# Performance work log

Hardware: AMD Instinct MI355X
Metric: run time of the kernel (lower is better)

## Reference

```python
import jax, jax.numpy as jnp
import numpy as np

DIM = 384
HEADS = 6
K = 10          # default k of DynamicGraphAttention
HID = 1536      # int(dim * mlp_ratio)
LN_EPS = 1e-5


def layernorm(x, g, b):
    m = jnp.mean(x, -1, keepdims=True)
    var = jnp.mean((x - m) ** 2, -1, keepdims=True)
    return (x - m) * jax.lax.rsqrt(var + LN_EPS) * g + b


def setup_inputs() -> dict:
    key = jax.random.key(0)
    ks = jax.random.split(key, 12)
    B, N, M, C = 16, 1024, 512, DIM
    s = 0.02
    return dict(
        q=jax.random.normal(ks[0], (B, N, C), jnp.float32),
        v=jax.random.normal(ks[1], (B, M, C), jnp.float32),
        q_pos=jax.random.normal(ks[2], (B, N, 3), jnp.float32),
        v_pos=jax.random.normal(ks[3], (B, M, 3), jnp.float32),
        norm1_g=jnp.ones((C,), jnp.float32), norm1_b=jnp.zeros((C,), jnp.float32),
        qkv_w=jax.random.normal(ks[4], (C, 3 * C), jnp.float32) * s,  # qkv_bias=False
        proj_w=jax.random.normal(ks[5], (C, C), jnp.float32) * s,
        proj_b=jnp.zeros((C,), jnp.float32),
        normq_g=jnp.ones((C,), jnp.float32), normq_b=jnp.zeros((C,), jnp.float32),
        normv_g=jnp.ones((C,), jnp.float32), normv_b=jnp.zeros((C,), jnp.float32),
        knn_w=jax.random.normal(ks[6], (2 * C, C), jnp.float32) * s,
        knn_b=jnp.zeros((C,), jnp.float32),
        norm2_g=jnp.ones((C,), jnp.float32), norm2_b=jnp.zeros((C,), jnp.float32),
        fc1_w=jax.random.normal(ks[7], (C, HID), jnp.float32) * s,
        fc1_b=jnp.zeros((HID,), jnp.float32),
        fc2_w=jax.random.normal(ks[8], (HID, C), jnp.float32) * s,
        fc2_b=jnp.zeros((C,), jnp.float32),
    )


def reference(q, v, q_pos, v_pos,
              norm1_g, norm1_b, qkv_w, proj_w, proj_b,
              normq_g, normq_b, normv_g, normv_b, knn_w, knn_b,
              norm2_g, norm2_b, fc1_w, fc1_b, fc2_w, fc2_b):
    B, N, C = q.shape
    D = C // HEADS

    # --- multi-head self-attention with pre-norm residual ---
    x = layernorm(q, norm1_g, norm1_b)
    qkv = (x @ qkv_w).reshape(B, N, 3, HEADS, D)
    qh, kh, vh = qkv[:, :, 0], qkv[:, :, 1], qkv[:, :, 2]   # [B,N,H,D]
    attn = jnp.einsum('bnhd,bmhd->bhnm', qh, kh) * (D ** -0.5)
    attn = jax.nn.softmax(attn, axis=-1)
    sa = jnp.einsum('bhnm,bmhd->bnhd', attn, vh).reshape(B, N, C)
    sa = sa @ proj_w + proj_b
    q = q + sa

    # --- dynamic graph cross-attention (knn gather + diff-concat MLP + max) ---
    nq = layernorm(q, normq_g, normq_b)          # [B,N,C]
    nv = layernorm(v, normv_g, normv_b)          # [B,M,C]
    # squared distances between query and kv positions: [B,N,M]
    d = (jnp.sum(q_pos ** 2, -1)[:, :, None]
         + jnp.sum(v_pos ** 2, -1)[:, None, :]
         - 2.0 * jnp.einsum('bnc,bmc->bnm', q_pos, v_pos))
    _, idx = jax.lax.top_k(-d, K)                # K nearest neighbors, [B,N,K]
    local_v = jax.vmap(lambda vv, ii: vv[ii])(nv, idx)   # [B,N,K,C]
    qe = nq[:, :, None, :]                                # [B,N,1,C]
    feat = jnp.concatenate(
        [local_v - qe, jnp.broadcast_to(qe, local_v.shape)], axis=-1)  # [B,N,K,2C]
    g = jax.nn.leaky_relu(feat @ knn_w + knn_b, negative_slope=0.2)
    q = q + jnp.max(g, axis=-2)                  # max over K neighbors

    # --- MLP with pre-norm residual ---
    h = layernorm(q, norm2_g, norm2_b)
    h = jax.nn.gelu(h @ fc1_w + fc1_b, approximate=False)
    h = h @ fc2_w + fc2_b
    return q + h
```

## Files before the change

kernel.cpp:

```cpp
#include <hip/hip_runtime.h>
#include <hip/hip_bf16.h>

#define CDIM 384
#define NHEAD 6
#define DHEAD 64
#define BB 16
#define NQ 1024
#define MV 512
#define HIDD 1536
#define KNN 10

typedef __attribute__((ext_vector_type(8))) __bf16 bf16x8;
typedef __attribute__((ext_vector_type(4))) float f32x4;
typedef __attribute__((ext_vector_type(4))) short short4v;

__device__ inline void ln_row(const float* __restrict__ xr, const float* __restrict__ gw,
                              const float* __restrict__ bw, __hip_bfloat16* __restrict__ outr,
                              int lane) {
  float v0[6];
  float s = 0.f;
#pragma unroll
  for (int i = 0; i < 3; i++) {
    float2 t = *reinterpret_cast<const float2*>(xr + i * 128 + lane * 2);
    v0[i * 2] = t.x; v0[i * 2 + 1] = t.y; s += t.x + t.y;
  }
  for (int off = 32; off; off >>= 1) s += __shfl_xor(s, off);
  float mean = s * (1.f / 384.f);
  float sq = 0.f;
#pragma unroll
  for (int i = 0; i < 6; i++) { float d = v0[i] - mean; sq += d * d; }
  for (int off = 32; off; off >>= 1) sq += __shfl_xor(sq, off);
  float rstd = rsqrtf(sq * (1.f / 384.f) + 1e-5f);
#pragma unroll
  for (int i = 0; i < 3; i++) {
    int c = i * 128 + lane * 2;
    float2 gg = *reinterpret_cast<const float2*>(gw + c);
    float2 bb = *reinterpret_cast<const float2*>(bw + c);
    __hip_bfloat162 p;
    p.x = __float2bfloat16((v0[i * 2] - mean) * rstd * gg.x + bb.x);
    p.y = __float2bfloat16((v0[i * 2 + 1] - mean) * rstd * gg.y + bb.y);
    *reinterpret_cast<__hip_bfloat162*>(outr + c) = p;
  }
}

__global__ __launch_bounds__(256) void prep_kernel(
    const float* __restrict__ qkv_w, const float* __restrict__ proj_w,
    const float* __restrict__ knn_w, const float* __restrict__ fc1_w,
    const float* __restrict__ fc2_w, const float* __restrict__ q,
    const float* __restrict__ g1, const float* __restrict__ b1,
    __hip_bfloat16* __restrict__ Wqkv_t, __hip_bfloat16* __restrict__ Wproj_t,
    __hip_bfloat16* __restrict__ W1_t, __hip_bfloat16* __restrict__ Wd_t,
    __hip_bfloat16* __restrict__ Wfc1_t, __hip_bfloat16* __restrict__ Wfc2_t,
    __hip_bfloat16* __restrict__ Xbf) {
  int gid = blockIdx.x;
  if (gid >= 1872) {
    int wave = (gid - 1872) * 4 + ((int)threadIdx.x >> 6);
    int lane = threadIdx.x & 63;
    ln_row(q + (size_t)wave * CDIM, g1, b1, Xbf + (size_t)wave * CDIM, lane);
    return;
  }
  __shared__ float t1[32][33];
  __shared__ float t2[32][33];
  int tx = threadIdx.x & 31, ty = (int)threadIdx.x >> 5;
  if (gid >= 576 && gid < 720) {
    int id = gid - 576;
    int k0 = (id % 12) * 32, n0 = (id / 12) * 32;
#pragma unroll
    for (int i = 0; i < 4; i++) {
      int k = k0 + ty + i * 8;
      float w1 = knn_w[(size_t)k * CDIM + n0 + tx];
      float w2 = knn_w[(size_t)(CDIM + k) * CDIM + n0 + tx];
      t1[ty + i * 8][tx] = w1;
      t2[ty + i * 8][tx] = w2 - w1;
    }
    __syncthreads();
#pragma unroll
    for (int i = 0; i < 4; i++) {
      W1_t[(size_t)(n0 + ty + i * 8) * CDIM + k0 + tx] = __float2bfloat16(t1[tx][ty + i * 8]);
      Wd_t[(size_t)(n0 + ty + i * 8) * CDIM + k0 + tx] = __float2bfloat16(t2[tx][ty + i * 8]);
    }
    return;
  }
  const float* W;
  __hip_bfloat16* Wt;
  int Kd, Nd, k0, n0;
  if (gid < 432) {
    W = qkv_w; Wt = Wqkv_t; Kd = 384; Nd = 1152;
    k0 = (gid % 12) * 32; n0 = (gid / 12) * 32;
  } else if (gid < 576) {
    int id = gid - 432;
    W = proj_w; Wt = Wproj_t; Kd = 384; Nd = 384;
    k0 = (id % 12) * 32; n0 = (id / 12) * 32;
  } else if (gid < 1296) {
    int id = gid - 720;
    W = fc1_w; Wt = Wfc1_t; Kd = 384; Nd = 1536;
    k0 = (id % 12) * 32; n0 = (id / 12) * 32;
  } else {
    int id = gid - 1296;
    W = fc2_w; Wt = Wfc2_t; Kd = 1536; Nd = 384;
    k0 = (id % 48) * 32; n0 = (id / 48) * 32;
  }
#pragma unroll
  for (int i = 0; i < 4; i++)
    t1[ty + i * 8][tx] = W[(size_t)(k0 + ty + i * 8) * Nd + n0 + tx];
  __syncthreads();
#pragma unroll
  for (int i = 0; i < 4; i++)
    Wt[(size_t)(n0 + ty + i * 8) * Kd + k0 + tx] = __float2bfloat16(t1[tx][ty + i * 8]);
}

__global__ __launch_bounds__(256) void ln_dual_kernel(const float* __restrict__ q1,
                                                      const float* __restrict__ v,
                                                      const float* __restrict__ gq,
                                                      const float* __restrict__ bq,
                                                      const float* __restrict__ gv,
                                                      const float* __restrict__ bv,
                                                      __hip_bfloat16* __restrict__ Xbf,
                                                      __hip_bfloat16* __restrict__ NV) {
  int wave = (int)((blockIdx.x * blockDim.x + threadIdx.x) >> 6);
  int lane = threadIdx.x & 63;
  if (wave < BB * NQ) {
    ln_row(q1 + (size_t)wave * CDIM, gq, bq, Xbf + (size_t)wave * CDIM, lane);
  } else {
    int r = wave - BB * NQ;
    ln_row(v + (size_t)r * CDIM, gv, bv, NV + (size_t)r * CDIM, lane);
  }
}

template <int EPI, int BM>
__global__ __launch_bounds__(256) void gemm_kernel(const __hip_bfloat16* __restrict__ A,
                                                   const __hip_bfloat16* __restrict__ Bt,
                                                   const float* __restrict__ bias,
                                                   const float* __restrict__ resid,
                                                   void* __restrict__ outp,
                                                   void* __restrict__ out2,
                                                   void* __restrict__ out3,
                                                   int M, int N, int Kdim) {
  constexpr int MI = BM / 32;
  constexpr int STAGEB = BM * 64 * 2 + 128 * 64 * 2;
  constexpr int SMEMB = (EPI == 5) ? (128 * 136 * 2 > STAGEB ? 128 * 136 * 2 : STAGEB) : STAGEB;
  __shared__ __align__(16) char smem[SMEMB];
  char* AsB = smem;
  char* BsB = smem + BM * 64 * 2;
  int m0 = blockIdx.y * BM, n0 = blockIdx.x * 128;
  const __hip_bfloat16* Ause = A;
  const __hip_bfloat16* Bt_use = Bt;
  bool isA1 = false;
  if (EPI == 6) {
    constexpr int A2B = 16384 / BM;
    if ((int)blockIdx.y >= A2B) {
      isA1 = true;
      m0 = (blockIdx.y - A2B) * BM;
      Ause = (const __hip_bfloat16*)out3;
    } else {
      Bt_use = Bt + (size_t)384 * 384;
    }
  }
  int t = threadIdx.x;
  int lane = t & 63, w = t >> 6;
  int wrow = w >> 1, wcol = w & 1;
  int lg = lane >> 4, lr = lane & 15;
  int gcol = (((lane & 7) ^ (lane >> 3)) * 8);
  const __hip_bfloat16* Ab = Ause + (size_t)(m0 + w * 8 + (lane >> 3)) * Kdim + gcol;
  const __hip_bfloat16* Bb = Bt_use + (size_t)(n0 + w * 8 + (lane >> 3)) * Kdim + gcol;
  f32x4 acc[MI][4] = {};
  for (int k0 = 0; k0 < Kdim; k0 += 64) {
    if (k0) __syncthreads();
#pragma unroll
    for (int i = 0; i < MI; i++)
      __builtin_amdgcn_global_load_lds(
          (const __attribute__((address_space(1))) void*)(Ab + (size_t)(i * 32) * Kdim + k0),
          (__attribute__((address_space(3))) void*)(AsB + (i * 4 + w) * 1024), 16, 0, 0);
#pragma unroll
    for (int i = 0; i < 4; i++)
      __builtin_amdgcn_global_load_lds(
          (const __attribute__((address_space(1))) void*)(Bb + (size_t)(i * 32) * Kdim + k0),
          (__attribute__((address_space(3))) void*)(BsB + (i * 4 + w) * 1024), 16, 0, 0);
    __syncthreads();
#pragma unroll
    for (int kk = 0; kk < 2; kk++) {
      bf16x8 a[MI], b[4];
#pragma unroll
      for (int i = 0; i < MI; i++) {
        int ra = wrow * (BM / 2) + i * 16 + lr;
        int sw = (((kk << 2) | lg) ^ (lr & 7)) * 16;
        a[i] = *reinterpret_cast<const bf16x8*>(AsB + ra * 128 + sw);
      }
#pragma unroll
      for (int j = 0; j < 4; j++) {
        int rb = wcol * 64 + j * 16 + lr;
        int sw = (((kk << 2) | lg) ^ (lr & 7)) * 16;
        b[j] = *reinterpret_cast<const bf16x8*>(BsB + rb * 128 + sw);
      }
#pragma unroll
      for (int i = 0; i < MI; i++)
#pragma unroll
        for (int j = 0; j < 4; j++)
          acc[i][j] = __builtin_amdgcn_mfma_f32_16x16x32_bf16(a[i], b[j], acc[i][j], 0, 0, 0);
    }
  }
  if (EPI == 5 && blockIdx.x >= 6) {
    __syncthreads();
    __hip_bfloat16* S = (__hip_bfloat16*)smem;
#pragma unroll
    for (int i = 0; i < MI; i++)
#pragma unroll
      for (int j = 0; j < 4; j++) {
        int lc = wcol * 64 + j * 16 + lr;
#pragma unroll
        for (int r = 0; r < 4; r++) {
          int lrow = wrow * 64 + i * 16 + lg * 4 + r;
          S[lc * 136 + lrow] = __float2bfloat16(acc[i][j][r]);
        }
      }
    __syncthreads();
    int b = m0 >> 10, nbase = m0 & 1023;
    int lc = t >> 1, half = t & 1;
    int c = n0 + lc - 2 * CDIM;
    int h = c >> 6, d = c & 63;
    __hip_bfloat16* dst = (__hip_bfloat16*)out3 +
                          ((size_t)((b * NHEAD + h) * DHEAD + d)) * NQ + nbase + half * 64;
#pragma unroll
    for (int u = 0; u < 8; u++)
      *reinterpret_cast<uint4*>(dst + u * 8) =
          *reinterpret_cast<const uint4*>(&S[lc * 136 + half * 64 + u * 8]);
    return;
  }
#pragma unroll
  for (int i = 0; i < MI; i++)
#pragma unroll
    for (int j = 0; j < 4; j++) {
      int col = n0 + wcol * 64 + j * 16 + lr;
#pragma unroll
      for (int r = 0; r < 4; r++) {
        int row = m0 + wrow * (BM / 2) + i * 16 + lg * 4 + r;
        float v = acc[i][j][r];
        if (EPI == 5) {
          int b = row >> 10, n = row & 1023;
          if (col < CDIM) {
            int h = col >> 6, d = col & 63;
            ((__hip_bfloat16*)outp)[(((size_t)(b * NHEAD + h)) * NQ + n) * DHEAD + d] =
                __float2bfloat16(v * 0.18033688f);
          } else {
            int c = col - CDIM, h = c >> 6, d = c & 63;
            ((__hip_bfloat16*)out2)[(((size_t)(b * NHEAD + h)) * NQ + n) * DHEAD + d] =
                __float2bfloat16(v);
          }
        } else if (EPI == 6) {
          float vv = v;
          if (!isA1) vv += bias[col];
          float* dst = isA1 ? (float*)out2 : (float*)outp;
          dst[(size_t)row * 384 + col] = vv;
        } else {
          if (EPI == 1 || EPI == 2 || EPI == 3) v += bias[col];
          if (EPI == 2) v += resid[(size_t)row * N + col];
          if (EPI == 3) v = 0.5f * v * (1.f + erff(v * 0.70710678118654752f));
          if (EPI == 0 || EPI == 3)
            ((__hip_bfloat16*)outp)[(size_t)row * N + col] = __float2bfloat16(v);
          else
            ((float*)outp)[(size_t)row * N + col] = v;
        }
      }
    }
}

__global__ __launch_bounds__(256) void attn_kernel(const __hip_bfloat16* __restrict__ Qb,
                                                   const __hip_bfloat16* __restrict__ Kb,
                                                   const __hip_bfloat16* __restrict__ Vt,
                                                   __hip_bfloat16* __restrict__ SAb) {
  __shared__ __align__(16) __hip_bfloat16 Ks[2][64][72];
  __shared__ __align__(16) __hip_bfloat16 Vs[2][64][72];
  int bh = blockIdx.x % 96;
  int qblk = blockIdx.x / 96;
  int t = threadIdx.x;
  int w = t >> 6, lane = t & 63;
  int lg = lane >> 4, lr = lane & 15;
  const __hip_bfloat16* Qp = Qb + (size_t)bh * NQ * DHEAD;
  const __hip_bfloat16* Kp = Kb + (size_t)bh * NQ * DHEAD;
  const __hip_bfloat16* Vp = Vt + (size_t)bh * DHEAD * NQ;
  int q0 = qblk * 128 + w * 32;
  bf16x8 qf[2][2];
#pragma unroll
  for (int qt = 0; qt < 2; qt++)
#pragma unroll
    for (int kk = 0; kk < 2; kk++)
      qf[qt][kk] = *reinterpret_cast<const bf16x8*>(
          Qp + (size_t)(q0 + qt * 16 + lr) * DHEAD + kk * 32 + lg * 8);
  int srow = w * 16 + (lane >> 2);
  int scol = (lane & 3) * 16;
  uint4 kr0 = *reinterpret_cast<const uint4*>(Kp + (size_t)srow * DHEAD + scol);
  uint4 kr1 = *reinterpret_cast<const uint4*>(Kp + (size_t)srow * DHEAD + scol + 8);
  uint4 vr0 = *reinterpret_cast<const uint4*>(Vp + (size_t)srow * NQ + scol);
  uint4 vr1 = *reinterpret_cast<const uint4*>(Vp + (size_t)srow * NQ + scol + 8);
  *reinterpret_cast<uint4*>(&Ks[0][srow][scol]) = kr0;
  *reinterpret_cast<uint4*>(&Ks[0][srow][scol + 8]) = kr1;
  *reinterpret_cast<uint4*>(&Vs[0][srow][scol]) = vr0;
  *reinterpret_cast<uint4*>(&Vs[0][srow][scol + 8]) = vr1;
  f32x4 o[2][4] = {};
  float l_[2] = {0.f, 0.f};
  __syncthreads();
  for (int kt = 0; kt < 16; kt++) {
    int cur = kt & 1;
    if (kt < 15) {
      int kb = (kt + 1) * 64;
      kr0 = *reinterpret_cast<const uint4*>(Kp + (size_t)(kb + srow) * DHEAD + scol);
      kr1 = *reinterpret_cast<const uint4*>(Kp + (size_t)(kb + srow) * DHEAD + scol + 8);
      vr0 = *reinterpret_cast<const uint4*>(Vp + (size_t)srow * NQ + kb + scol);
      vr1 = *reinterpret_cast<const uint4*>(Vp + (size_t)srow * NQ + kb + scol + 8);
    }
    f32x4 s[4][2] = {};
#pragma unroll
    for (int kti = 0; kti < 4; kti++)
#pragma unroll
      for (int kk = 0; kk < 2; kk++) {
        bf16x8 a = *reinterpret_cast<const bf16x8*>(&Ks[cur][kti * 16 + lr][kk * 32 + lg * 8]);
#pragma unroll
        for (int qt = 0; qt < 2; qt++)
          s[kti][qt] = __builtin_amdgcn_mfma_f32_16x16x32_bf16(a, qf[qt][kk], s[kti][qt], 0, 0, 0);
      }
#pragma unroll
    for (int qt = 0; qt < 2; qt++) {
      float ls = 0.f;
#pragma unroll
      for (int kti = 0; kti < 4; kti++) {
        float p0 = __builtin_amdgcn_exp2f(s[kti][qt][0]);
        float p1 = __builtin_amdgcn_exp2f(s[kti][qt][1]);
        float p2 = __builtin_amdgcn_exp2f(s[kti][qt][2]);
        float p3 = __builtin_amdgcn_exp2f(s[kti][qt][3]);
        s[kti][qt][0] = p0; s[kti][qt][1] = p1; s[kti][qt][2] = p2; s[kti][qt][3] = p3;
        ls += (p0 + p1) + (p2 + p3);
      }
      l_[qt] += ls;
    }
#pragma unroll
    for (int kti = 0; kti < 4; kti++) {
      short4v pa[2];
#pragma unroll
      for (int qt = 0; qt < 2; qt++) {
#pragma unroll
        for (int r = 0; r < 4; r++) {
          __bf16 hv = (__bf16)s[kti][qt][r];
          pa[qt][r] = __builtin_bit_cast(short, hv);
        }
      }
#pragma unroll
      for (int dt = 0; dt < 4; dt++) {
        short4v vb = *reinterpret_cast<const short4v*>(&Vs[cur][dt * 16 + lr][kti * 16 + lg * 4]);
#pragma unroll
        for (int qt = 0; qt < 2; qt++)
          o[qt][dt] = __builtin_amdgcn_mfma_f32_16x16x16bf16_1k(pa[qt], vb, o[qt][dt], 0, 0, 0);
      }
    }
    if (kt < 15) {
      int nb = cur ^ 1;
      *reinterpret_cast<uint4*>(&Ks[nb][srow][scol]) = kr0;
      *reinterpret_cast<uint4*>(&Ks[nb][srow][scol + 8]) = kr1;
      *reinterpret_cast<uint4*>(&Vs[nb][srow][scol]) = vr0;
      *reinterpret_cast<uint4*>(&Vs[nb][srow][scol + 8]) = vr1;
      __syncthreads();
    }
  }
#pragma unroll
  for (int qt = 0; qt < 2; qt++) {
    l_[qt] += __shfl_xor(l_[qt], 16);
    l_[qt] += __shfl_xor(l_[qt], 32);
  }
  int b = bh / NHEAD, h = bh % NHEAD;
#pragma unroll
  for (int qt = 0; qt < 2; qt++)
#pragma unroll
    for (int r = 0; r < 4; r++) {
      float li = __shfl(l_[qt], (lane & 48) | (((lane >> 4) & 3) * 4 + r));
      float inv = 1.f / li;
      int row = q0 + qt * 16 + ((lane >> 4) & 3) * 4 + r;
#pragma unroll
      for (int dt = 0; dt < 4; dt++)
        SAb[((size_t)(b * NQ + row)) * CDIM + h * DHEAD + dt * 16 + lr] =
            __float2bfloat16(o[qt][dt][r] * inv);
    }
}

__global__ __launch_bounds__(256) void knn_fused_kernel(const float* __restrict__ q_pos,
                                                        const float* __restrict__ v_pos,
                                                        const float* __restrict__ A1,
                                                        const float* __restrict__ A2,
                                                        const float* __restrict__ q1,
                                                        const float* __restrict__ g2,
                                                        const float* __restrict__ b2,
                                                        float* __restrict__ q2,
                                                        __hip_bfloat16* __restrict__ xout) {
  int wq = (int)((blockIdx.x * blockDim.x + threadIdx.x) >> 6);
  int lane = threadIdx.x & 63;
  if (wq >= BB * NQ) return;
  int b = wq >> 10;
  const float* qp = q_pos + (size_t)wq * 3;
  float qx = qp[0], qy = qp[1], qz = qp[2];
  float qs = qx * qx + qy * qy + qz * qz;
  unsigned long long pk[8];
#pragma unroll
  for (int j = 0; j < 8; j++) {
    int m = lane + 64 * j;
    const float* vp = v_pos + ((size_t)b * MV + m) * 3;
    float vx = vp[0], vy = vp[1], vz = vp[2];
    float vs = vx * vx + vy * vy + vz * vz;
    float d = qs + vs - 2.f * (qx * vx + qy * vy + qz * vz);
    unsigned ub = __float_as_uint(d);
    ub ^= (unsigned)(((int)ub >> 31)) | 0x80000000u;
    pk[j] = ((unsigned long long)ub << 32) | (unsigned)m;
  }
  unsigned long long lm = pk[0];
#pragma unroll
  for (int j = 1; j < 8; j++) lm = pk[j] < lm ? pk[j] : lm;
  int idxs[KNN];
#pragma unroll
  for (int k = 0; k < KNN; k++) {
    unsigned long long bm = lm;
#pragma unroll
    for (int off = 1; off < 64; off <<= 1) {
      unsigned long long ot = __shfl_xor(bm, off);
      bm = ot < bm ? ot : bm;
    }
    int widx = (int)(unsigned)(bm & 0xFFFFFFFFull);
    idxs[k] = widx;
    if ((widx & 63) == lane) {
      int jj = widx >> 6;
#pragma unroll
      for (int j = 0; j < 8; j++)
        if (j == jj) pk[j] = ~0ull;
      lm = pk[0];
#pragma unroll
      for (int j = 1; j < 8; j++) lm = pk[j] < lm ? pk[j] : lm;
    }
  }
  float a2[6], mx[6];
#pragma unroll
  for (int i = 0; i < 6; i++) {
    a2[i] = A2[(size_t)wq * CDIM + lane + 64 * i];
    mx[i] = -1e30f;
  }
#pragma unroll
  for (int k = 0; k < KNN; k++) {
    const float* a1 = A1 + ((size_t)b * MV + idxs[k]) * CDIM;
#pragma unroll
    for (int i = 0; i < 6; i++) {
      float g = a1[lane + 64 * i] + a2[i];
      g = g > 0.f ? g : 0.2f * g;
      mx[i] = fmaxf(mx[i], g);
    }
  }
  float vals[6];
  float s = 0.f;
#pragma unroll
  for (int i = 0; i < 6; i++) {
    vals[i] = q1[(size_t)wq * CDIM + lane + 64 * i] + mx[i];
    s += vals[i];
  }
  for (int off = 32; off; off >>= 1) s += __shfl_xor(s, off);
  float mean = s * (1.f / 384.f);
  float sq = 0.f;
#pragma unroll
  for (int i = 0; i < 6; i++) { float d = vals[i] - mean; sq += d * d; }
  for (int off = 32; off; off >>= 1) sq += __shfl_xor(sq, off);
  float rstd = rsqrtf(sq * (1.f / 384.f) + 1e-5f);
#pragma unroll
  for (int i = 0; i < 6; i++) {
    int c = lane + 64 * i;
    q2[(size_t)wq * CDIM + c] = vals[i];
    xout[(size_t)wq * CDIM + c] = __float2bfloat16((vals[i] - mean) * rstd * g2[c] + b2[c]);
  }
}

extern "C" void kernel_launch(void* const* d_in, const int* in_sizes, int n_in,
                              void* d_out, int out_size, void* d_ws, size_t ws_size,
                              hipStream_t stream) {
  const float* q = (const float*)d_in[0];
  const float* v = (const float*)d_in[1];
  const float* q_pos = (const float*)d_in[2];
  const float* v_pos = (const float*)d_in[3];
  const float* norm1_g = (const float*)d_in[4];
  const float* norm1_b = (const float*)d_in[5];
  const float* qkv_w = (const float*)d_in[6];
  const float* proj_w = (const float*)d_in[7];
  const float* proj_b = (const float*)d_in[8];
  const float* normq_g = (const float*)d_in[9];
  const float* normq_b = (const float*)d_in[10];
  const float* normv_g = (const float*)d_in[11];
  const float* normv_b = (const float*)d_in[12];
  const float* knn_w = (const float*)d_in[13];
  const float* knn_b = (const float*)d_in[14];
  const float* norm2_g = (const float*)d_in[15];
  const float* norm2_b = (const float*)d_in[16];
  const float* fc1_w = (const float*)d_in[17];
  const float* fc1_b = (const float*)d_in[18];
  const float* fc2_w = (const float*)d_in[19];
  const float* fc2_b = (const float*)d_in[20];

  char* ws = (char*)d_ws;
  const size_t SZ_Wqkv = (size_t)1152 * 384 * 2;
  const size_t SZ_W384 = (size_t)384 * 384 * 2;
  const size_t SZ_Wfc = (size_t)1536 * 384 * 2;
  const size_t SZ_Xbf = (size_t)16384 * 384 * 2;
  const size_t SZ_QKV = (size_t)16384 * 1152 * 2;
  const size_t SZ_q32 = (size_t)16384 * 384 * 4;
  const size_t SZ_NV = (size_t)8192 * 384 * 2;

  size_t o_Wqkv = 0;
  size_t o_Wproj = o_Wqkv + SZ_Wqkv;
  size_t o_W1 = o_Wproj + SZ_W384;
  size_t o_Wd = o_W1 + SZ_W384;
  size_t o_Wfc1 = o_Wd + SZ_W384;
  size_t o_Wfc2 = o_Wfc1 + SZ_Wfc;
  size_t o_Xbf = o_Wfc2 + SZ_Wfc;
  size_t o_QKV = o_Xbf + SZ_Xbf;
  size_t o_A1 = o_QKV;
  size_t o_A2 = o_QKV + (size_t)8192 * 384 * 4;
  size_t o_Qb = o_QKV + SZ_QKV;
  size_t o_Kb = o_Qb + SZ_Xbf;
  size_t o_Vt = o_Kb + SZ_Xbf;
  size_t o_SA = o_Vt + SZ_Xbf;
  size_t o_H1 = o_Qb;
  size_t o_q1 = o_SA + SZ_Xbf;
  size_t o_NV = o_q1 + SZ_q32;
  size_t o_q2 = o_NV + SZ_NV;

  __hip_bfloat16* Wqkv_t = (__hip_bfloat16*)(ws + o_Wqkv);
  __hip_bfloat16* Wproj_t = (__hip_bfloat16*)(ws + o_Wproj);
  __hip_bfloat16* W1_t = (__hip_bfloat16*)(ws + o_W1);
  __hip_bfloat16* Wd_t = (__hip_bfloat16*)(ws + o_Wd);
  __hip_bfloat16* Wfc1_t = (__hip_bfloat16*)(ws + o_Wfc1);
  __hip_bfloat16* Wfc2_t = (__hip_bfloat16*)(ws + o_Wfc2);
  __hip_bfloat16* Xbf = (__hip_bfloat16*)(ws + o_Xbf);
  float* A1f = (float*)(ws + o_A1);
  float* A2f = (float*)(ws + o_A2);
  __hip_bfloat16* Qb = (__hip_bfloat16*)(ws + o_Qb);
  __hip_bfloat16* Kb = (__hip_bfloat16*)(ws + o_Kb);
  __hip_bfloat16* Vt = (__hip_bfloat16*)(ws + o_Vt);
  __hip_bfloat16* SAb = (__hip_bfloat16*)(ws + o_SA);
  __hip_bfloat16* H1 = (__hip_bfloat16*)(ws + o_H1);
  float* q1 = (float*)(ws + o_q1);
  __hip_bfloat16* NV = (__hip_bfloat16*)(ws + o_NV);
  float* q2 = (float*)(ws + o_q2);
  float* outf = (float*)d_out;

  prep_kernel<<<5968, 256, 0, stream>>>(qkv_w, proj_w, knn_w, fc1_w, fc2_w, q,
                                        norm1_g, norm1_b,
                                        Wqkv_t, Wproj_t, W1_t, Wd_t, Wfc1_t, Wfc2_t, Xbf);
  gemm_kernel<5, 128><<<dim3(9, 128), 256, 0, stream>>>(Xbf, Wqkv_t, nullptr, nullptr,
                                                        Qb, Kb, Vt, 16384, 1152, 384);
  attn_kernel<<<768, 256, 0, stream>>>(Qb, Kb, Vt, SAb);
  gemm_kernel<2, 64><<<dim3(3, 256), 256, 0, stream>>>(SAb, Wproj_t, proj_b, q, q1,
                                                       nullptr, nullptr, 16384, 384, 384);
  ln_dual_kernel<<<6144, 256, 0, stream>>>(q1, v, normq_g, normq_b, normv_g, normv_b, Xbf, NV);
  gemm_kernel<6, 64><<<dim3(3, 384), 256, 0, stream>>>(Xbf, W1_t, knn_b, nullptr, A2f,
                                                       A1f, (void*)NV, 16384, 384, 384);
  knn_fused_kernel<<<4096, 256, 0, stream>>>(q_pos, v_pos, A1f, A2f, q1,
                                             norm2_g, norm2_b, q2, Xbf);
  gemm_kernel<3, 128><<<dim3(12, 128), 256, 0, stream>>>(Xbf, Wfc1_t, fc1_b, nullptr, H1,
                                                         nullptr, nullptr, 16384, 1536, 384);
  gemm_kernel<2, 64><<<dim3(3, 256), 256, 0, stream>>>(H1, Wfc2_t, fc2_b, q2, outf,
                                                       nullptr, nullptr, 16384, 384, 1536);
}
```

Before: 270.4 us.

## Move kNN top-k, value layernorm and neighbour GEMM into earlier kernels

The kNN distance computation and top-k selection now run as extra blocks in the prep kernel, which writes the indices to a workspace buffer that the fused kNN kernel reads back. The value-side layernorm also moves into the prep kernel. The nv@W1 GEMM moves into the QKV GEMM launch as extra grid rows, so only the query-side GEMM is left after the residual. The aim is to put work that does not depend on the attention output onto earlier, larger launches, and to shorten the serial chain after attention. The cost is an extra index buffer round trip through global memory and a larger prep grid with mixed block roles.

```diff
diff --git a/kernel.cpp b/kernel.cpp
--- a/kernel.cpp
+++ b/kernel.cpp
@@ -48,11 +48,64 @@
     const float* __restrict__ knn_w, const float* __restrict__ fc1_w,
     const float* __restrict__ fc2_w, const float* __restrict__ q,
     const float* __restrict__ g1, const float* __restrict__ b1,
+    const float* __restrict__ v, const float* __restrict__ gv, const float* __restrict__ bv,
+    const float* __restrict__ q_pos, const float* __restrict__ v_pos,
     __hip_bfloat16* __restrict__ Wqkv_t, __hip_bfloat16* __restrict__ Wproj_t,
     __hip_bfloat16* __restrict__ W1_t, __hip_bfloat16* __restrict__ Wd_t,
     __hip_bfloat16* __restrict__ Wfc1_t, __hip_bfloat16* __restrict__ Wfc2_t,
-    __hip_bfloat16* __restrict__ Xbf) {
+    __hip_bfloat16* __restrict__ Xbf, __hip_bfloat16* __restrict__ NV,
+    int* __restrict__ idxb) {
   int gid = blockIdx.x;
+  if (gid >= 8016) {
+    int wq = (gid - 8016) * 4 + ((int)threadIdx.x >> 6);
+    int lane = threadIdx.x & 63;
+    int b = wq >> 10;
+    const float* qp = q_pos + (size_t)wq * 3;
+    float qx = qp[0], qy = qp[1], qz = qp[2];
+    float qs = qx * qx + qy * qy + qz * qz;
+    unsigned long long pk[8];
+#pragma unroll
+    for (int j = 0; j < 8; j++) {
+      int m = lane + 64 * j;
+      const float* vp = v_pos + ((size_t)b * MV + m) * 3;
+      float vx = vp[0], vy = vp[1], vz = vp[2];
+      float vs = vx * vx + vy * vy + vz * vz;
+      float d = qs + vs - 2.f * (qx * vx + qy * vy + qz * vz);
+      unsigned ub = __float_as_uint(d);
+      ub ^= (unsigned)(((int)ub >> 31)) | 0x80000000u;
+      pk[j] = ((unsigned long long)ub << 32) | (unsigned)m;
+    }
+    unsigned long long lm = pk[0];
+#pragma unroll
+    for (int j = 1; j < 8; j++) lm = pk[j] < lm ? pk[j] : lm;
+#pragma unroll
+    for (int k = 0; k < KNN; k++) {
+      unsigned long long bm = lm;
+#pragma unroll
+      for (int off = 1; off < 64; off <<= 1) {
+        unsigned long long ot = __shfl_xor(bm, off);
+        bm = ot < bm ? ot : bm;
+      }
+      int widx = (int)(unsigned)(bm & 0xFFFFFFFFull);
+      if (lane == 0) idxb[wq * KNN + k] = widx;
+      if ((widx & 63) == lane) {
+        int jj = widx >> 6;
+#pragma unroll
+        for (int j = 0; j < 8; j++)
+          if (j == jj) pk[j] = ~0ull;
+        lm = pk[0];
+#pragma unroll
+        for (int j = 1; j < 8; j++) lm = pk[j] < lm ? pk[j] : lm;
+      }
+    }
+    return;
+  }
+  if (gid >= 5968) {
+    int row = (gid - 5968) * 4 + ((int)threadIdx.x >> 6);
+    int lane = threadIdx.x & 63;
+    ln_row(v + (size_t)row * CDIM, gv, bv, NV + (size_t)row * CDIM, lane);
+    return;
+  }
   if (gid >= 1872) {
     int wave = (gid - 1872) * 4 + ((int)threadIdx.x >> 6);
     int lane = threadIdx.x & 63;
@@ -109,22 +162,14 @@
     Wt[(size_t)(n0 + ty + i * 8) * Kd + k0 + tx] = __float2bfloat16(t1[tx][ty + i * 8]);
 }
 
-__global__ __launch_bounds__(256) void ln_dual_kernel(const float* __restrict__ q1,
-                                                      const float* __restrict__ v,
-                                                      const float* __restrict__ gq,
-                                                      const float* __restrict__ bq,
-                                                      const float* __restrict__ gv,
-                                                      const float* __restrict__ bv,
-                                                      __hip_bfloat16* __restrict__ Xbf,
-                                                      __hip_bfloat16* __restrict__ NV) {
+__global__ __launch_bounds__(256) void ln_kernel(const float* __restrict__ x,
+                                                 const float* __restrict__ gw,
+                                                 const float* __restrict__ bw,
+                                                 __hip_bfloat16* __restrict__ out, int rows) {
   int wave = (int)((blockIdx.x * blockDim.x + threadIdx.x) >> 6);
   int lane = threadIdx.x & 63;
-  if (wave < BB * NQ) {
-    ln_row(q1 + (size_t)wave * CDIM, gq, bq, Xbf + (size_t)wave * CDIM, lane);
-  } else {
-    int r = wave - BB * NQ;
-    ln_row(v + (size_t)r * CDIM, gv, bv, NV + (size_t)r * CDIM, lane);
-  }
+  if (wave >= rows) return;
+  ln_row(x + (size_t)wave * CDIM, gw, bw, out + (size_t)wave * CDIM, lane);
 }
 
 template <int EPI, int BM>
@@ -146,6 +191,15 @@
   const __hip_bfloat16* Ause = A;
   const __hip_bfloat16* Bt_use = Bt;
   bool isA1 = false;
+  if (EPI == 5) {
+    if ((int)blockIdx.y >= 128) {
+      if ((int)blockIdx.x >= 3) return;
+      isA1 = true;
+      m0 = (blockIdx.y - 128) * 128;
+      Ause = (const __hip_bfloat16*)bias;
+      Bt_use = Bt + (size_t)(1152 * 384 + 384 * 384);
+    }
+  }
   if (EPI == 6) {
     constexpr int A2B = 16384 / BM;
     if ((int)blockIdx.y >= A2B) {
@@ -199,7 +253,7 @@
           acc[i][j] = __builtin_amdgcn_mfma_f32_16x16x32_bf16(a[i], b[j], acc[i][j], 0, 0, 0);
     }
   }
-  if (EPI == 5 && blockIdx.x >= 6) {
+  if (EPI == 5 && !isA1 && blockIdx.x >= 6) {
     __syncthreads();
     __hip_bfloat16* S = (__hip_bfloat16*)smem;
 #pragma unroll
@@ -236,15 +290,19 @@
         int row = m0 + wrow * (BM / 2) + i * 16 + lg * 4 + r;
         float v = acc[i][j][r];
         if (EPI == 5) {
-          int b = row >> 10, n = row & 1023;
-          if (col < CDIM) {
-            int h = col >> 6, d = col & 63;
-            ((__hip_bfloat16*)outp)[(((size_t)(b * NHEAD + h)) * NQ + n) * DHEAD + d] =
-                __float2bfloat16(v * 0.18033688f);
+          if (isA1) {
+            ((float*)(size_t)resid)[(size_t)row * 384 + col] = v;
           } else {
-            int c = col - CDIM, h = c >> 6, d = c & 63;
-            ((__hip_bfloat16*)out2)[(((size_t)(b * NHEAD + h)) * NQ + n) * DHEAD + d] =
-                __float2bfloat16(v);
+            int b = row >> 10, n = row & 1023;
+            if (col < CDIM) {
+              int h = col >> 6, d = col & 63;
+              ((__hip_bfloat16*)outp)[(((size_t)(b * NHEAD + h)) * NQ + n) * DHEAD + d] =
+                  __float2bfloat16(v * 0.18033688f);
+            } else {
+              int c = col - CDIM, h = c >> 6, d = c & 63;
+              ((__hip_bfloat16*)out2)[(((size_t)(b * NHEAD + h)) * NQ + n) * DHEAD + d] =
+                  __float2bfloat16(v);
+            }
           }
         } else if (EPI == 6) {
           float vv = v;
@@ -380,8 +438,7 @@
     }
 }
 
-__global__ __launch_bounds__(256) void knn_fused_kernel(const float* __restrict__ q_pos,
-                                                        const float* __restrict__ v_pos,
+__global__ __launch_bounds__(256) void knn_fused_kernel(const int* __restrict__ idxb,
                                                         const float* __restrict__ A1,
                                                         const float* __restrict__ A2,
                                                         const float* __restrict__ q1,
@@ -393,45 +450,9 @@
   int lane = threadIdx.x & 63;
   if (wq >= BB * NQ) return;
   int b = wq >> 10;
-  const float* qp = q_pos + (size_t)wq * 3;
-  float qx = qp[0], qy = qp[1], qz = qp[2];
-  float qs = qx * qx + qy * qy + qz * qz;
-  unsigned long long pk[8];
-#pragma unroll
-  for (int j = 0; j < 8; j++) {
-    int m = lane + 64 * j;
-    const float* vp = v_pos + ((size_t)b * MV + m) * 3;
-    float vx = vp[0], vy = vp[1], vz = vp[2];
-    float vs = vx * vx + vy * vy + vz * vz;
-    float d = qs + vs - 2.f * (qx * vx + qy * vy + qz * vz);
-    unsigned ub = __float_as_uint(d);
-    ub ^= (unsigned)(((int)ub >> 31)) | 0x80000000u;
-    pk[j] = ((unsigned long long)ub << 32) | (unsigned)m;
-  }
-  unsigned long long lm = pk[0];
-#pragma unroll
-  for (int j = 1; j < 8; j++) lm = pk[j] < lm ? pk[j] : lm;
   int idxs[KNN];
 #pragma unroll
-  for (int k = 0; k < KNN; k++) {
-    unsigned long long bm = lm;
-#pragma unroll
-    for (int off = 1; off < 64; off <<= 1) {
-      unsigned long long ot = __shfl_xor(bm, off);
-      bm = ot < bm ? ot : bm;
-    }
-    int widx = (int)(unsigned)(bm & 0xFFFFFFFFull);
-    idxs[k] = widx;
-    if ((widx & 63) == lane) {
-      int jj = widx >> 6;
-#pragma unroll
-      for (int j = 0; j < 8; j++)
-        if (j == jj) pk[j] = ~0ull;
-      lm = pk[0];
-#pragma unroll
-      for (int j = 1; j < 8; j++) lm = pk[j] < lm ? pk[j] : lm;
-    }
-  }
+  for (int k = 0; k < KNN; k++) idxs[k] = idxb[wq * KNN + k];
   float a2[6], mx[6];
 #pragma unroll
   for (int i = 0; i < 6; i++) {
@@ -522,6 +543,7 @@
   size_t o_q1 = o_SA + SZ_Xbf;
   size_t o_NV = o_q1 + SZ_q32;
   size_t o_q2 = o_NV + SZ_NV;
+  size_t o_idx = o_q2 + SZ_q32;
 
   __hip_bfloat16* Wqkv_t = (__hip_bfloat16*)(ws + o_Wqkv);
   __hip_bfloat16* Wproj_t = (__hip_bfloat16*)(ws + o_Wproj);
@@ -540,20 +562,24 @@
   float* q1 = (float*)(ws + o_q1);
   __hip_bfloat16* NV = (__hip_bfloat16*)(ws + o_NV);
   float* q2 = (float*)(ws + o_q2);
+  int* idxb = (int*)(ws + o_idx);
   float* outf = (float*)d_out;
 
-  prep_kernel<<<5968, 256, 0, stream>>>(qkv_w, proj_w, knn_w, fc1_w, fc2_w, q,
-                                        norm1_g, norm1_b,
-                                        Wqkv_t, Wproj_t, W1_t, Wd_t, Wfc1_t, Wfc2_t, Xbf);
-  gemm_kernel<5, 128><<<dim3(9, 128), 256, 0, stream>>>(Xbf, Wqkv_t, nullptr, nullptr,
+  prep_kernel<<<12112, 256, 0, stream>>>(qkv_w, proj_w, knn_w, fc1_w, fc2_w, q,
+                                         norm1_g, norm1_b, v, normv_g, normv_b,
+                                         q_pos, v_pos,
+                                         Wqkv_t, Wproj_t, W1_t, Wd_t, Wfc1_t, Wfc2_t,
+                                         Xbf, NV, idxb);
+  gemm_kernel<5, 128><<<dim3(9, 192), 256, 0, stream>>>(Xbf, Wqkv_t,
+                                                        (const float*)NV, (const float*)A1f,
                                                         Qb, Kb, Vt, 16384, 1152, 384);
   attn_kernel<<<768, 256, 0, stream>>>(Qb, Kb, Vt, SAb);
   gemm_kernel<2, 64><<<dim3(3, 256), 256, 0, stream>>>(SAb, Wproj_t, proj_b, q, q1,
                                                        nullptr, nullptr, 16384, 384, 384);
-  ln_dual_kernel<<<6144, 256, 0, stream>>>(q1, v, normq_g, normq_b, normv_g, normv_b, Xbf, NV);
-  gemm_kernel<6, 64><<<dim3(3, 384), 256, 0, stream>>>(Xbf, W1_t, knn_b, nullptr, A2f,
-                                                       A1f, (void*)NV, 16384, 384, 384);
-  knn_fused_kernel<<<4096, 256, 0, stream>>>(q_pos, v_pos, A1f, A2f, q1,
+  ln_kernel<<<4096, 256, 0, stream>>>(q1, normq_g, normq_b, Xbf, 16384);
+  gemm_kernel<1, 64><<<dim3(3, 256), 256, 0, stream>>>(Xbf, Wd_t, knn_b, nullptr, A2f,
+                                                       nullptr, nullptr, 16384, 384, 384);
+  knn_fused_kernel<<<4096, 256, 0, stream>>>(idxb, A1f, A2f, q1,
                                              norm2_g, norm2_b, q2, Xbf);
   gemm_kernel<3, 128><<<dim3(12, 128), 256, 0, stream>>>(Xbf, Wfc1_t, fc1_b, nullptr, H1,
                                                          nullptr, nullptr, 16384, 1536, 384);
```

After: 282.9 us. 1.05x slower.
